# Performance work log

Measured on AMD Instinct MI355X. Metric: run time of the kernel, lower is better.

Reference implementation:

```python
import jax, jax.numpy as jnp
import numpy as np

B, L, V, E = 8, 2000, 50000, 300      # batch, doc len, vocab, embed dim
NL, LW = 8922, 10                     # num labels, words per label desc
F_, K, H = 200, 10, 200               # num_filters, kernel_size, label_hidden
FEAT = E + H                          # feat_size = 500


def setup_inputs():
    key = jax.random.key(0)
    ks = jax.random.split(key, 12)
    n = lambda k, sh, s=0.02: jax.random.normal(k, sh, jnp.float32) * s
    x = jax.random.randint(ks[0], (B, L), 0, V)
    y = (jax.random.uniform(ks[1], (B, NL)) < 0.01).astype(jnp.float32)
    mask = jnp.ones((B, L), jnp.float32)
    word_emb = n(ks[2], (V, E), 0.1)
    label_idx_matrix = jax.random.randint(ks[3], (NL, LW), 0, V)
    label_idx_mask = jnp.ones((NL, LW), jnp.float32)
    adj_matrix = (jax.random.uniform(ks[4], (NL, NL)) < 0.002).astype(jnp.float32)
    num_neighbors = jnp.maximum(adj_matrix.sum(axis=1), 1.0)
    return {
        'x': x, 'y': y, 'mask': mask,
        'word_emb': word_emb,
        'label_idx_matrix': label_idx_matrix,
        'label_idx_mask': label_idx_mask,
        'adj_matrix': adj_matrix,
        'num_neighbors': num_neighbors,
        'Wg': n(ks[5], (E, H)), 'bg': jnp.zeros((H,), jnp.float32),
        'Wc': n(ks[6], (F_, E, K)), 'bc': jnp.zeros((F_,), jnp.float32),
        'Wp': n(ks[7], (F_, E)), 'bp': jnp.zeros((E,), jnp.float32),
        'Wo': n(ks[8], (F_, FEAT)), 'bo': jnp.zeros((FEAT,), jnp.float32),
    }


def reference(x, y, mask, word_emb, label_idx_matrix, label_idx_mask,
              adj_matrix, num_neighbors, Wg, bg, Wc, bc, Wp, bp, Wo, bo):
    # --- average label embedding over label description words ---
    le = word_emb[label_idx_matrix]                              # [NL, LW, E]
    avg = (le * label_idx_mask[..., None]).sum(1)
    avg = avg / label_idx_mask.sum(axis=-1, keepdims=True)       # [NL, E]
    # --- conv graph encoder over label hierarchy ---
    agg = (adj_matrix @ avg) / num_neighbors[:, None]            # [NL, E]
    gh = jax.nn.relu(agg @ Wg + bg)                              # [NL, H]
    graph_emb = jnp.concatenate([avg, gh], axis=-1)              # [NL, FEAT]
    # --- document encoding (dropouts are identity in eval) ---
    xe = word_emb[x] * mask[..., None]                           # [B, L, E]
    c = jax.lax.conv_general_dilated(
        xe.transpose(0, 2, 1), Wc, window_strides=(1,), padding='VALID',
        dimension_numbers=('NCH', 'OIH', 'NCH')) + bc[None, :, None]
    c = jax.nn.relu(c).transpose(0, 2, 1)                        # [B, Lp, F]
    pj = jnp.tanh(c @ Wp + bp)                                   # [B, Lp, E]
    # --- label-wise attention ---
    scores = jnp.einsum('ble,ne->bnl', pj, avg)                  # [B, NL, Lp]
    attn = jax.nn.softmax(scores, axis=-1)
    attn_out = jnp.einsum('bnl,blf->bnf', attn, c)               # [B, NL, F]
    proj = jax.nn.relu(attn_out @ Wo + bo)                       # [B, NL, FEAT]
    logits = (graph_emb[None] * proj).sum(-1)                    # [B, NL]
    # --- BCE-with-logits (sum) / batch ---
    bce = jnp.maximum(logits, 0.0) - logits * y + jnp.log1p(jnp.exp(-jnp.abs(logits)))
    loss = bce.sum() / B
    return (logits, loss)
```

## Files before the change

### kernel.cpp

```cpp
#include <hip/hip_runtime.h>
#include <math.h>

#define B_    8
#define L_    2000
#define V_    50000
#define E_    300
#define NL_   8922
#define NLP_  8960
#define LW_   10
#define F_    200
#define KW_   10
#define H_    200
#define FEAT_ 500
#define LP_   1991

typedef __attribute__((ext_vector_type(8))) short bf16x8;
typedef __attribute__((ext_vector_type(4))) float f32x4;

static __device__ __forceinline__ unsigned short f2b(float f) {
  unsigned u = __builtin_bit_cast(unsigned, f);
  u += 0x7FFF + ((u >> 16) & 1);
  return (unsigned short)(u >> 16);
}
static __device__ __forceinline__ float b2f(unsigned short u) {
  unsigned v = ((unsigned)u) << 16;
  return __builtin_bit_cast(float, v);
}
static __device__ __forceinline__ float fast_tanh(float x) {
  x = fminf(fmaxf(x, -10.f), 10.f);
  float t = __expf(2.f * x);
  return (t - 1.f) / (t + 1.f);
}

#define MFMA(a, b, c) __builtin_amdgcn_mfma_f32_16x16x32_bf16(a, b, c, 0, 0, 0)


__global__ __launch_bounds__(256) void k_avg(const float* __restrict__ we,
                                             const int* __restrict__ lidx,
                                             const float* __restrict__ lmask,
                                             float* __restrict__ avg,
                                             unsigned short* __restrict__ avgb,
                                             unsigned short* __restrict__ geb) {
  int idx = blockIdx.x * 256 + threadIdx.x;
  if (idx >= NLP_ * 80) return;
  int n = idx / 80, e4 = idx - n * 80;
  if (n >= NL_ || e4 >= 75) {
    *(ushort4*)&avgb[(size_t)n * 320 + e4 * 4] = make_ushort4(0, 0, 0, 0);
    return;
  }
  float ax = 0.f, ay = 0.f, az = 0.f, aw = 0.f, ms = 0.f;
#pragma unroll
  for (int w = 0; w < LW_; ++w) {
    float mw = lmask[n * LW_ + w];
    const float4 f = *(const float4*)&we[(size_t)lidx[n * LW_ + w] * E_ + e4 * 4];
    ax = fmaf(f.x, mw, ax); ay = fmaf(f.y, mw, ay);
    az = fmaf(f.z, mw, az); aw = fmaf(f.w, mw, aw);
    ms += mw;
  }
  float inv = 1.f / ms;
  float4 v = {ax * inv, ay * inv, az * inv, aw * inv};
  *(float4*)&avg[(size_t)n * 300 + e4 * 4] = v;
  ushort4 ub = make_ushort4(f2b(v.x), f2b(v.y), f2b(v.z), f2b(v.w));
  *(ushort4*)&avgb[(size_t)n * 320 + e4 * 4] = ub;
  *(ushort4*)&geb[(size_t)n * 512 + e4 * 4] = ub;
}

__global__ __launch_bounds__(256) void k_agg(const float* __restrict__ adj,
                                             const float* __restrict__ avg,
                                             const float* __restrict__ nnb,
                                             float* __restrict__ agg) {
  __shared__ int s_idx[1024];
  __shared__ float s_val[1024];
  __shared__ int s_cnt;
  const int n = blockIdx.x;
  const int tid = threadIdx.x;
  if (tid == 0) s_cnt = 0;
  __syncthreads();
  const float* row = adj + (size_t)n * NL_;
  for (int j = tid; j < NL_; j += 256) {
    float v = row[j];
    if (v != 0.f) {
      int p = atomicAdd(&s_cnt, 1);
      if (p < 1024) { s_idx[p] = j; s_val[p] = v; }
    }
  }
  __syncthreads();
  const int m = min(s_cnt, 1024);
  const float inv = 1.f / nnb[n];
  float a0 = 0.f, a1 = 0.f;
  for (int i = 0; i < m; ++i) {
    const float* ar = avg + (size_t)s_idx[i] * 300;
    float v = s_val[i];
    a0 = fmaf(v, ar[tid], a0);
    if (tid < E_ - 256) a1 = fmaf(v, ar[tid + 256], a1);
  }
  agg[(size_t)n * E_ + tid] = a0 * inv;
  if (tid < E_ - 256) agg[(size_t)n * E_ + tid + 256] = a1 * inv;
}

__global__ __launch_bounds__(256) void k_gh(const float* __restrict__ agg,
                                            const float* __restrict__ Wg,
                                            const float* __restrict__ bg,
                                            unsigned short* __restrict__ geb) {
  __shared__ float s_agg[2400];
  const int n0 = blockIdx.x * 8;
  const int tid = threadIdx.x;
  for (int i = tid; i < 2400; i += 256) {
    int e = i >> 3, nn = i & 7;
    int n = n0 + nn;
    s_agg[i] = (n < NL_) ? agg[(size_t)n * E_ + e] : 0.f;
  }
  __syncthreads();
  if (tid < 96) {
    int nn = tid / 12, c = tid - nn * 12;
    int n = n0 + nn;
    if (n < NL_) geb[(size_t)n * 512 + 500 + c] = 0;
  }
  if (tid < H_) {
    const int h = tid;
    float bb = bg[h];
    float acc[8];
#pragma unroll
    for (int i = 0; i < 8; ++i) acc[i] = bb;
    for (int e = 0; e < E_; ++e) {
      float w = Wg[(size_t)e * H_ + h];
      float4 a0 = *(const float4*)&s_agg[e * 8];
      float4 a1 = *(const float4*)&s_agg[e * 8 + 4];
      acc[0] = fmaf(a0.x, w, acc[0]); acc[1] = fmaf(a0.y, w, acc[1]);
      acc[2] = fmaf(a0.z, w, acc[2]); acc[3] = fmaf(a0.w, w, acc[3]);
      acc[4] = fmaf(a1.x, w, acc[4]); acc[5] = fmaf(a1.y, w, acc[5]);
      acc[6] = fmaf(a1.z, w, acc[6]); acc[7] = fmaf(a1.w, w, acc[7]);
    }
#pragma unroll
    for (int i = 0; i < 8; ++i) {
      int n = n0 + i;
      if (n < NL_) geb[(size_t)n * 512 + 300 + h] = f2b(fmaxf(acc[i], 0.f));
    }
  }
}

__global__ __launch_bounds__(256) void k_wct(const float* __restrict__ Wc,
                                             unsigned short* __restrict__ WcF) {
  int idx = blockIdx.x * 256 + threadIdx.x;
  if (idx >= KW_ * 16 * 10 * 512) return;
  int koff = idx / (16 * 10 * 512);
  int rem = idx - koff * (16 * 10 * 512);
  int ft = rem / (10 * 512);
  int rem2 = rem - ft * (10 * 512);
  int ks = rem2 >> 9;
  int t = rem2 & 511;
  int lane = t >> 3, j = t & 7;
  int f = ft * 16 + (lane & 15);
  int e = ks * 32 + (lane >> 4) * 8 + j;
  float v = (f < F_ && e < E_) ? Wc[((size_t)f * E_ + e) * KW_ + koff] : 0.f;
  WcF[idx] = f2b(v);
}

__global__ __launch_bounds__(256) void k_wpt(const float* __restrict__ Wp,
                                             unsigned short* __restrict__ WpF) {
  int idx = blockIdx.x * 256 + threadIdx.x;
  if (idx >= 20 * 7 * 512) return;
  int et = idx / (7 * 512);
  int rem = idx - et * (7 * 512);
  int kt = rem >> 9;
  int t = rem & 511;
  int lane = t >> 3, j = t & 7;
  int e = et * 16 + (lane & 15);
  int f = kt * 32 + (lane >> 4) * 8 + j;
  float v = (e < E_ && f < F_) ? Wp[(size_t)f * E_ + e] : 0.f;
  WpF[idx] = f2b(v);
}

__global__ __launch_bounds__(256) void k_wot(const float* __restrict__ Wo,
                                             unsigned short* __restrict__ WoF) {
  int idx = blockIdx.x * 256 + threadIdx.x;
  if (idx >= 32 * 7 * 512) return;
  int g = idx / (7 * 512);
  int rem = idx - g * (7 * 512);
  int kt = rem >> 9;
  int t = rem & 511;
  int lane = t >> 3, j = t & 7;
  int feat = (g >> 3) * 128 + (g & 7) * 16 + (lane & 15);
  int f = kt * 32 + (lane >> 4) * 8 + j;
  float v = (feat < FEAT_ && f < F_) ? Wo[(size_t)f * FEAT_ + feat] : 0.f;
  WoF[idx] = f2b(v);
}

__global__ __launch_bounds__(256) void k_cpj(const int* __restrict__ x,
                                             const float* __restrict__ mask,
                                             const float* __restrict__ we,
                                             const unsigned short* __restrict__ WcF,
                                             const float* __restrict__ bc,
                                             const unsigned short* __restrict__ WpF,
                                             const float* __restrict__ bp,
                                             unsigned short* __restrict__ cF,
                                             unsigned short* __restrict__ pjF) {
  __shared__ __attribute__((aligned(16))) unsigned char smem[78896];
  unsigned short* s_xe  = (unsigned short*)smem;
  unsigned short* s_pjF = (unsigned short*)smem;
  unsigned short* s_cA  = (unsigned short*)(smem + 50224);

  const int b = blockIdx.y;
  const int l0 = blockIdx.x * 64;
  const int tid = threadIdx.x;
  const int wv = tid >> 6, lane = tid & 63, quad = lane >> 4, c16 = lane & 15;

  for (int i = tid; i < 73 * 75; i += 256) {
    int row = i / 75, e4 = i - row * 75;
    int l = l0 + row;
    float4 v = {0.f, 0.f, 0.f, 0.f};
    if (l < L_) {
      int bl = b * L_ + l;
      v = *(const float4*)&we[(size_t)x[bl] * E_ + e4 * 4];
      float mm = mask[bl];
      v.x *= mm; v.y *= mm; v.z *= mm; v.w *= mm;
    }
    *(ushort4*)&s_xe[row * 344 + e4 * 4] =
        make_ushort4(f2b(v.x), f2b(v.y), f2b(v.z), f2b(v.w));
  }
  for (int i = tid; i < 73 * 5; i += 256) {
    int row = i / 5, c = i - row * 5;
    *(ushort4*)&s_xe[row * 344 + (75 + c) * 4] = make_ushort4(0, 0, 0, 0);
  }
  __syncthreads();

  f32x4 acc[4][4];
#pragma unroll
  for (int mt = 0; mt < 4; ++mt)
#pragma unroll
    for (int j = 0; j < 4; ++j) acc[mt][j] = (f32x4){0.f, 0.f, 0.f, 0.f};
  for (int koff = 0; koff < KW_; ++koff) {
#pragma unroll
    for (int ks = 0; ks < 10; ++ks) {
      bf16x8 a[4];
#pragma unroll
      for (int mt = 0; mt < 4; ++mt)
        a[mt] = *(const bf16x8*)&s_xe[(mt * 16 + c16 + koff) * 344 + ks * 32 + quad * 8];
#pragma unroll
      for (int jj = 0; jj < 4; ++jj) {
        bf16x8 bw = *(const bf16x8*)
            &WcF[(((size_t)((koff * 16 + wv * 4 + jj) * 10 + ks)) << 9) + (lane << 3)];
#pragma unroll
        for (int mt = 0; mt < 4; ++mt) acc[mt][jj] = MFMA(a[mt], bw, acc[mt][jj]);
      }
    }
  }
  unsigned short* cFb = cF + (size_t)b * (16 * 64 * 512);
#pragma unroll
  for (int jj = 0; jj < 4; ++jj) {
    const int ft2 = wv * 4 + jj;
    const int f = ft2 * 16 + c16;
    const float bcv = (f < F_) ? bc[f] : 0.f;
    const int kt = ft2 >> 1;
    const int qA = ((ft2 & 1) << 1) | (c16 >> 3);
    const int jA = c16 & 7;
#pragma unroll
    for (int mt = 0; mt < 4; ++mt) {
      unsigned short u[4];
#pragma unroll
      for (int r = 0; r < 4; ++r) u[r] = f2b(fmaxf(acc[mt][jj][r] + bcv, 0.f));
      int su = (l0 >> 5) + (mt >> 1);
      int lane_c = ((((mt & 1) << 1) | (quad >> 1)) << 4) + c16;
      *(ushort4*)&cFb[(((size_t)(ft2 * 64 + su)) << 9) + lane_c * 8 + ((quad & 1) << 2)] =
          make_ushort4(u[0], u[1], u[2], u[3]);
      if (ft2 < 14) {
#pragma unroll
        for (int r = 0; r < 4; ++r)
          s_cA[(((size_t)(mt * 7 + kt)) << 9) + ((qA << 4) + quad * 4 + r) * 8 + jA] = u[r];
      }
    }
  }
  __syncthreads();

  f32x4 pacc[4][5];
#pragma unroll
  for (int mt = 0; mt < 4; ++mt)
#pragma unroll
    for (int j = 0; j < 5; ++j) pacc[mt][j] = (f32x4){0.f, 0.f, 0.f, 0.f};
#pragma unroll
  for (int kt = 0; kt < 7; ++kt) {
    bf16x8 a[4];
#pragma unroll
    for (int mt = 0; mt < 4; ++mt)
      a[mt] = *(const bf16x8*)&s_cA[(((size_t)(mt * 7 + kt)) << 9) + (lane << 3)];
#pragma unroll
    for (int j = 0; j < 5; ++j) {
      bf16x8 bw = *(const bf16x8*)
          &WpF[(((size_t)((wv * 5 + j) * 7 + kt)) << 9) + (lane << 3)];
#pragma unroll
      for (int mt = 0; mt < 4; ++mt) pacc[mt][j] = MFMA(a[mt], bw, pacc[mt][j]);
    }
  }
  __syncthreads();
#pragma unroll
  for (int j = 0; j < 5; ++j) {
    const int et = wv * 5 + j;
    const int e = et * 16 + c16;
    const float bpe = (e < E_) ? bp[e] : 0.f;
    const int ks = et >> 1;
    const int qP = ((et & 1) << 1) | (c16 >> 3);
    const int jP = c16 & 7;
#pragma unroll
    for (int mt = 0; mt < 4; ++mt) {
#pragma unroll
      for (int r = 0; r < 4; ++r) {
        float v = (e < E_) ? fast_tanh(pacc[mt][j][r] + bpe) : 0.f;
        s_pjF[(((size_t)(mt * 10 + ks)) << 9) + ((qP << 4) + quad * 4 + r) * 8 + jP] = f2b(v);
      }
    }
  }
  __syncthreads();
  {
    unsigned short* dst = pjF + (((size_t)((b * 128 + (l0 >> 4)) * 10)) << 9);
    for (int i = tid; i < 2560; i += 256)
      *(uint4*)&dst[i * 8] = *(const uint4*)&s_pjF[i * 8];
  }
}

__global__ __launch_bounds__(256, 2) void k_attn(
    const unsigned short* __restrict__ pjF,
    const unsigned short* __restrict__ cF,
    const unsigned short* __restrict__ avgb,
    const unsigned short* __restrict__ WoF,
    const unsigned short* __restrict__ geb,
    const float* __restrict__ bo,
    float* __restrict__ out) {
  __shared__ __attribute__((aligned(16))) unsigned char smem[58880];
  unsigned short* s_avgF = (unsigned short*)smem;
  unsigned short* s_AOF  = (unsigned short*)smem;
  unsigned short* s_PF   = (unsigned short*)(smem + 40960);
  float* s_wsum = (float*)(smem + 57344);
  float* s_sum  = (float*)(smem + 58368);
  float* s_lg   = (float*)(smem + 58624);

  const int tid = threadIdx.x;
  const int b  = blockIdx.x & 7;
  const int n0 = (blockIdx.x >> 3) << 6;
  const int wv = tid >> 6, lane = tid & 63, quad = lane >> 4, c16 = lane & 15;

  if (tid < 64) s_lg[tid] = 0.f;
  for (int i = tid; i < 2560; i += 256) {
    int nl = i / 40, eo = i - nl * 40;
    int lane_s = ((eo & 3) << 4) | (nl & 15);
    *(uint4*)&s_avgF[(((size_t)((eo >> 2) * 4 + (nl >> 4))) << 9) + lane_s * 8] =
        *(const uint4*)&avgb[(size_t)(n0 + nl) * 320 + eo * 8];
  }
  __syncthreads();

  const unsigned short* pjb = pjF + (size_t)b * (128 * 10 * 512);
  const unsigned short* cFb = cF + (size_t)b * (16 * 64 * 512);

  f32x4 o[4][4];
#pragma unroll
  for (int i = 0; i < 4; ++i)
#pragma unroll
    for (int j = 0; j < 4; ++j) o[i][j] = (f32x4){0.f, 0.f, 0.f, 0.f};
  float ssum[4] = {0.f, 0.f, 0.f, 0.f};

  for (int lc = 0; lc < 16; ++lc) {
    f32x4 accs[2][4];
#pragma unroll
    for (int mt = 0; mt < 2; ++mt)
#pragma unroll
      for (int nt = 0; nt < 4; ++nt) accs[mt][nt] = (f32x4){0.f, 0.f, 0.f, 0.f};
    {
      const unsigned short* pr =
          pjb + (((size_t)((lc * 8 + wv * 2) * 10)) << 9) + (lane << 3);
#pragma unroll
      for (int ks = 0; ks < 10; ++ks) {
        bf16x8 a0 = *(const bf16x8*)(pr + ((size_t)ks << 9));
        bf16x8 a1 = *(const bf16x8*)(pr + ((size_t)(10 + ks) << 9));
#pragma unroll
        for (int nt = 0; nt < 4; ++nt) {
          bf16x8 bb = *(const bf16x8*)&s_avgF[(((size_t)(ks * 4 + nt)) << 9) + (lane << 3)];
          accs[0][nt] = MFMA(a0, bb, accs[0][nt]);
          accs[1][nt] = MFMA(a1, bb, accs[1][nt]);
        }
      }
    }
    __syncthreads();
#pragma unroll
    for (int nt = 0; nt < 4; ++nt) {
      float psum = 0.f;
#pragma unroll
      for (int mt = 0; mt < 2; ++mt) {
        const int lb = (lc << 7) + wv * 32 + mt * 16 + quad * 4;
        unsigned short u[4];
#pragma unroll
        for (int r = 0; r < 4; ++r) {
          float p = (lb + r < LP_) ? __expf(accs[mt][nt][r]) : 0.f;
          psum += p;
          u[r] = f2b(p);
        }
        int lane_P = (((mt << 1) | (quad >> 1)) << 4) + c16;
        *(ushort4*)&s_PF[(((size_t)(nt * 4 + wv)) << 9) + lane_P * 8 + ((quad & 1) << 2)] =
            make_ushort4(u[0], u[1], u[2], u[3]);
      }
      psum += __shfl_xor(psum, 16);
      psum += __shfl_xor(psum, 32);
      ssum[nt] += psum;
    }
    __syncthreads();
    {
      const unsigned short* cw =
          cFb + (((size_t)(wv * 4 * 64 + lc * 4)) << 9) + (lane << 3);
#pragma unroll
      for (int sub = 0; sub < 4; ++sub) {
        bf16x8 ap[4];
#pragma unroll
        for (int nt = 0; nt < 4; ++nt)
          ap[nt] = *(const bf16x8*)&s_PF[(((size_t)(nt * 4 + sub)) << 9) + (lane << 3)];
#pragma unroll
        for (int ft = 0; ft < 4; ++ft) {
          bf16x8 bb = *(const bf16x8*)(cw + (((size_t)(ft * 64 + sub)) << 9));
#pragma unroll
          for (int nt = 0; nt < 4; ++nt) o[nt][ft] = MFMA(ap[nt], bb, o[nt][ft]);
        }
      }
    }
  }

  if (lane < 16) {
#pragma unroll
    for (int nt = 0; nt < 4; ++nt) s_wsum[wv * 64 + nt * 16 + lane] = ssum[nt];
  }
  __syncthreads();
  if (tid < 64)
    s_sum[tid] = s_wsum[tid] + s_wsum[64 + tid] + s_wsum[128 + tid] + s_wsum[192 + tid];
  __syncthreads();
#pragma unroll
  for (int nt = 0; nt < 4; ++nt) {
    float inv4[4];
#pragma unroll
    for (int r = 0; r < 4; ++r) inv4[r] = 1.f / s_sum[nt * 16 + quad * 4 + r];
#pragma unroll
    for (int ft = 0; ft < 4; ++ft) {
      int f = wv * 64 + ft * 16 + c16;
      if (f < 224) {
        int kt = f >> 5;
        int qA = (f & 31) >> 3;
        int jA = f & 7;
#pragma unroll
        for (int r = 0; r < 4; ++r)
          s_AOF[(((size_t)(nt * 7 + kt)) << 9) + ((qA << 4) + quad * 4 + r) * 8 + jA] =
              f2b(o[nt][ft][r] * inv4[r]);
      }
    }
  }
  __syncthreads();
  float la[4][4];
#pragma unroll
  for (int nt = 0; nt < 4; ++nt)
#pragma unroll
    for (int r = 0; r < 4; ++r) la[nt][r] = 0.f;
#pragma unroll
  for (int i = 0; i < 8; ++i) {
    f32x4 pa[4];
#pragma unroll
    for (int nt = 0; nt < 4; ++nt) pa[nt] = (f32x4){0.f, 0.f, 0.f, 0.f};
    const unsigned short* wof = WoF + (((size_t)((wv * 8 + i) * 7)) << 9) + (lane << 3);
#pragma unroll
    for (int kt = 0; kt < 7; ++kt) {
      bf16x8 bw = *(const bf16x8*)(wof + ((size_t)kt << 9));
#pragma unroll
      for (int nt = 0; nt < 4; ++nt) {
        bf16x8 aa = *(const bf16x8*)&s_AOF[(((size_t)(nt * 7 + kt)) << 9) + (lane << 3)];
        pa[nt] = MFMA(aa, bw, pa[nt]);
      }
    }
    int feat = wv * 128 + i * 16 + c16;
    float bof = (feat < FEAT_) ? bo[feat] : 0.f;
#pragma unroll
    for (int nt = 0; nt < 4; ++nt) {
#pragma unroll
      for (int r = 0; r < 4; ++r) {
        int ng = n0 + nt * 16 + quad * 4 + r;
        float pv = fmaxf(pa[nt][r] + bof, 0.f);
        float gv = (feat < FEAT_) ? b2f(geb[(size_t)ng * 512 + feat]) : 0.f;
        la[nt][r] = fmaf(pv, gv, la[nt][r]);
      }
    }
  }
#pragma unroll
  for (int nt = 0; nt < 4; ++nt)
#pragma unroll
    for (int r = 0; r < 4; ++r) {
      float v = la[nt][r];
      v += __shfl_xor(v, 1); v += __shfl_xor(v, 2);
      v += __shfl_xor(v, 4); v += __shfl_xor(v, 8);
      if (c16 == 0) atomicAdd(&s_lg[nt * 16 + quad * 4 + r], v);
    }
  __syncthreads();
  if (tid < 64) {
    int ng = n0 + tid;
    if (ng < NL_) out[(size_t)b * NL_ + ng] = s_lg[tid];
  }
}

__global__ __launch_bounds__(1024) void k_loss(const float* __restrict__ lgts,
                                               const float* __restrict__ y,
                                               float* __restrict__ loss) {
  __shared__ float red[1024];
  const int tid = threadIdx.x;
  float s = 0.f;
  for (int i = tid; i < B_ * NL_; i += 1024) {
    float l = lgts[i], yy = y[i];
    s += fmaxf(l, 0.f) - l * yy + log1pf(expf(-fabsf(l)));
  }
  red[tid] = s;
  __syncthreads();
  for (int st = 512; st > 0; st >>= 1) {
    if (tid < st) red[tid] += red[tid + st];
    __syncthreads();
  }
  if (tid == 0) loss[0] = red[0] * (1.f / B_);
}

extern "C" void kernel_launch(void* const* d_in, const int* in_sizes, int n_in,
                              void* d_out, int out_size, void* d_ws, size_t ws_size,
                              hipStream_t stream) {
  const int*   x     = (const int*)  d_in[0];
  const float* y     = (const float*)d_in[1];
  const float* mask  = (const float*)d_in[2];
  const float* we    = (const float*)d_in[3];
  const int*   lidx  = (const int*)  d_in[4];
  const float* lmask = (const float*)d_in[5];
  const float* adj   = (const float*)d_in[6];
  const float* nnb   = (const float*)d_in[7];
  const float* Wg    = (const float*)d_in[8];
  const float* bg    = (const float*)d_in[9];
  const float* Wc    = (const float*)d_in[10];
  const float* bc    = (const float*)d_in[11];
  const float* Wp    = (const float*)d_in[12];
  const float* bp    = (const float*)d_in[13];
  const float* Wo    = (const float*)d_in[14];
  const float* bo    = (const float*)d_in[15];
  float* out = (float*)d_out;
  char* W = (char*)d_ws;

  unsigned short* pjF  = (unsigned short*)(W + 0);
  unsigned short* cF   = (unsigned short*)(W + 10485760);
  unsigned short* avgb = (unsigned short*)(W + 18874368);
  unsigned short* geb  = (unsigned short*)(W + 24608768);
  float*          agg  = (float*)(W + 33783808);
  unsigned short* WcF  = (unsigned short*)(W + 44490208);
  unsigned short* WpF  = (unsigned short*)(W + 46128608);
  unsigned short* WoF  = (unsigned short*)(W + 46271968);
  float*          avg  = (float*)(W + 0);

  k_avg<<<(NLP_ * 80 + 255) / 256, 256, 0, stream>>>(we, lidx, lmask, avg, avgb, geb);
  k_agg<<<NL_, 256, 0, stream>>>(adj, avg, nnb, agg);
  k_gh<<<(NL_ + 7) / 8, 256, 0, stream>>>(agg, Wg, bg, geb);
  k_wct<<<(KW_ * 16 * 10 * 512 + 255) / 256, 256, 0, stream>>>(Wc, WcF);
  k_wpt<<<(20 * 7 * 512 + 255) / 256, 256, 0, stream>>>(Wp, WpF);
  k_wot<<<(32 * 7 * 512 + 255) / 256, 256, 0, stream>>>(Wo, WoF);
  k_cpj<<<dim3(32, B_), 256, 0, stream>>>(x, mask, we, WcF, bc, WpF, bp, cF, pjF);
  k_attn<<<140 * 8, 256, 0, stream>>>(pjF, cF, avgb, WoF, geb, bo, out);
  k_loss<<<1, 1024, 0, stream>>>(out, y, out + B_ * NL_);
}
```

Baseline: 1.237 ms.

## Restructure attention kernel with double-buffered LDS staging and per-wave label tiles

The attention kernel is reorganized so each wave owns 16 labels across the full feature width. The label-embedding operand is now held in registers instead of LDS. The pj and c tiles for each 32-position chunk are brought into LDS with global_load_lds, double-buffered so the next chunk loads while the current one is computed. The graph-embedding buffer gets an MFMA-fragment-friendly layout, so the epilogue reads it with one vector load per tile instead of scattered scalar loads. This also needs a memset of that buffer and matching index changes in k_avg, k_gh and k_wot. The aim is to remove redundant global reads and the cross-wave syncs, at the cost of more registers (14 accumulator tiles), more LDS, and a full-buffer waitcnt barrier every iteration.

```diff
diff --git a/kernel.cpp b/kernel.cpp
--- a/kernel.cpp
+++ b/kernel.cpp
@@ -31,6 +31,11 @@
   float t = __expf(2.f * x);
   return (t - 1.f) / (t + 1.f);
 }
+static __device__ __forceinline__ void stage16(const void* g, void* l) {
+  __builtin_amdgcn_global_load_lds(
+      (const __attribute__((address_space(1))) unsigned int*)g,
+      (__attribute__((address_space(3))) unsigned int*)l, 16, 0, 0);
+}
 
 #define MFMA(a, b, c) __builtin_amdgcn_mfma_f32_16x16x32_bf16(a, b, c, 0, 0, 0)
 
@@ -40,7 +45,7 @@
                                              const float* __restrict__ lmask,
                                              float* __restrict__ avg,
                                              unsigned short* __restrict__ avgb,
-                                             unsigned short* __restrict__ geb) {
+                                             unsigned short* __restrict__ geF) {
   int idx = blockIdx.x * 256 + threadIdx.x;
   if (idx >= NLP_ * 80) return;
   int n = idx / 80, e4 = idx - n * 80;
@@ -60,9 +65,15 @@
   float inv = 1.f / ms;
   float4 v = {ax * inv, ay * inv, az * inv, aw * inv};
   *(float4*)&avg[(size_t)n * 300 + e4 * 4] = v;
-  ushort4 ub = make_ushort4(f2b(v.x), f2b(v.y), f2b(v.z), f2b(v.w));
-  *(ushort4*)&avgb[(size_t)n * 320 + e4 * 4] = ub;
-  *(ushort4*)&geb[(size_t)n * 512 + e4 * 4] = ub;
+  *(ushort4*)&avgb[(size_t)n * 320 + e4 * 4] =
+      make_ushort4(f2b(v.x), f2b(v.y), f2b(v.z), f2b(v.w));
+  int ntg = n >> 4, quad = (n >> 2) & 3, r = n & 3;
+  int ftg = (e4 * 4) >> 4, c0 = (e4 * 4) & 15;
+  size_t tb = (((size_t)ntg * 32 + ftg) << 8);
+  float vv[4] = {v.x, v.y, v.z, v.w};
+#pragma unroll
+  for (int t = 0; t < 4; ++t)
+    geF[(tb + quad * 16 + c0 + t) * 4 + r] = f2b(vv[t]);
 }
 
 __global__ __launch_bounds__(256) void k_agg(const float* __restrict__ adj,
@@ -101,7 +112,7 @@
 __global__ __launch_bounds__(256) void k_gh(const float* __restrict__ agg,
                                             const float* __restrict__ Wg,
                                             const float* __restrict__ bg,
-                                            unsigned short* __restrict__ geb) {
+                                            unsigned short* __restrict__ geF) {
   __shared__ float s_agg[2400];
   const int n0 = blockIdx.x * 8;
   const int tid = threadIdx.x;
@@ -111,13 +122,9 @@
     s_agg[i] = (n < NL_) ? agg[(size_t)n * E_ + e] : 0.f;
   }
   __syncthreads();
-  if (tid < 96) {
-    int nn = tid / 12, c = tid - nn * 12;
-    int n = n0 + nn;
-    if (n < NL_) geb[(size_t)n * 512 + 500 + c] = 0;
-  }
   if (tid < H_) {
     const int h = tid;
+    const int feat = 300 + h;
     float bb = bg[h];
     float acc[8];
 #pragma unroll
@@ -131,10 +138,14 @@
       acc[4] = fmaf(a1.x, w, acc[4]); acc[5] = fmaf(a1.y, w, acc[5]);
       acc[6] = fmaf(a1.z, w, acc[6]); acc[7] = fmaf(a1.w, w, acc[7]);
     }
+    const int ftg = feat >> 4, cc = feat & 15;
 #pragma unroll
     for (int i = 0; i < 8; ++i) {
       int n = n0 + i;
-      if (n < NL_) geb[(size_t)n * 512 + 300 + h] = f2b(fmaxf(acc[i], 0.f));
+      if (n < NL_) {
+        size_t tb = (((size_t)(n >> 4) * 32 + ftg) << 8);
+        geF[(tb + ((n >> 2) & 3) * 16 + cc) * 4 + (n & 3)] = f2b(fmaxf(acc[i], 0.f));
+      }
     }
   }
 }
@@ -180,7 +191,7 @@
   int kt = rem >> 9;
   int t = rem & 511;
   int lane = t >> 3, j = t & 7;
-  int feat = (g >> 3) * 128 + (g & 7) * 16 + (lane & 15);
+  int feat = g * 16 + (lane & 15);
   int f = kt * 32 + (lane >> 4) * 8 + j;
   float v = (feat < FEAT_ && f < F_) ? Wo[(size_t)f * FEAT_ + feat] : 0.f;
   WoF[idx] = f2b(v);
@@ -322,16 +333,14 @@
     const unsigned short* __restrict__ cF,
     const unsigned short* __restrict__ avgb,
     const unsigned short* __restrict__ WoF,
-    const unsigned short* __restrict__ geb,
+    const unsigned short* __restrict__ geF,
     const float* __restrict__ bo,
     float* __restrict__ out) {
-  __shared__ __attribute__((aligned(16))) unsigned char smem[58880];
-  unsigned short* s_avgF = (unsigned short*)smem;
-  unsigned short* s_AOF  = (unsigned short*)smem;
-  unsigned short* s_PF   = (unsigned short*)(smem + 40960);
-  float* s_wsum = (float*)(smem + 57344);
-  float* s_sum  = (float*)(smem + 58368);
-  float* s_lg   = (float*)(smem + 58624);
+  __shared__ __attribute__((aligned(16))) unsigned char smem[74240];
+  unsigned short* Ps  = (unsigned short*)(smem + 69632);
+  float* s_sum = (float*)(smem + 73728);
+  float* s_lg  = (float*)(smem + 73984);
+  unsigned short* AOs = (unsigned short*)smem;
 
   const int tid = threadIdx.x;
   const int b  = blockIdx.x & 7;
@@ -339,145 +348,147 @@
   const int wv = tid >> 6, lane = tid & 63, quad = lane >> 4, c16 = lane & 15;
 
   if (tid < 64) s_lg[tid] = 0.f;
-  for (int i = tid; i < 2560; i += 256) {
-    int nl = i / 40, eo = i - nl * 40;
-    int lane_s = ((eo & 3) << 4) | (nl & 15);
-    *(uint4*)&s_avgF[(((size_t)((eo >> 2) * 4 + (nl >> 4))) << 9) + lane_s * 8] =
-        *(const uint4*)&avgb[(size_t)(n0 + nl) * 320 + eo * 8];
-  }
-  __syncthreads();
+
+  bf16x8 bavg[10];
+  {
+    const unsigned short* ab = avgb + (size_t)(n0 + wv * 16 + c16) * 320 + quad * 8;
+#pragma unroll
+    for (int ks = 0; ks < 10; ++ks) bavg[ks] = *(const bf16x8*)(ab + ks * 32);
+  }
 
   const unsigned short* pjb = pjF + (size_t)b * (128 * 10 * 512);
   const unsigned short* cFb = cF + (size_t)b * (16 * 64 * 512);
 
-  f32x4 o[4][4];
-#pragma unroll
-  for (int i = 0; i < 4; ++i)
-#pragma unroll
-    for (int j = 0; j < 4; ++j) o[i][j] = (f32x4){0.f, 0.f, 0.f, 0.f};
-  float ssum[4] = {0.f, 0.f, 0.f, 0.f};
-
-  for (int lc = 0; lc < 16; ++lc) {
-    f32x4 accs[2][4];
-#pragma unroll
-    for (int mt = 0; mt < 2; ++mt)
-#pragma unroll
-      for (int nt = 0; nt < 4; ++nt) accs[mt][nt] = (f32x4){0.f, 0.f, 0.f, 0.f};
+  {
+    const unsigned char* pg = (const unsigned char*)pjb;
+#pragma unroll
+    for (int t = 0; t < 5; ++t) {
+      int off = (wv * 5 + t) << 10;
+      stage16(pg + off + lane * 16, smem + off);
+    }
+#pragma unroll
+    for (int t = 0; t < 4; ++t) {
+      int ft = wv + t * 4;
+      if (ft < 14)
+        stage16((const unsigned char*)cFb + (((size_t)(ft * 64)) << 10) + lane * 16,
+                smem + 20480 + (ft << 10));
+    }
+  }
+
+  f32x4 o[14];
+#pragma unroll
+  for (int i = 0; i < 14; ++i) o[i] = (f32x4){0.f, 0.f, 0.f, 0.f};
+  float ssum = 0.f;
+
+  for (int lc = 0; lc < 64; ++lc) {
+    __builtin_amdgcn_s_waitcnt(0);
+    __syncthreads();
+    unsigned char* cur = smem + ((lc & 1) ? 34816 : 0);
+    unsigned char* nxt = smem + ((lc & 1) ? 0 : 34816);
+    if (lc + 1 < 64) {
+      const unsigned char* pg =
+          (const unsigned char*)pjb + (((size_t)((lc + 1) * 20)) << 10);
+#pragma unroll
+      for (int t = 0; t < 5; ++t) {
+        int off = (wv * 5 + t) << 10;
+        stage16(pg + off + lane * 16, nxt + off);
+      }
+#pragma unroll
+      for (int t = 0; t < 4; ++t) {
+        int ft = wv + t * 4;
+        if (ft < 14)
+          stage16((const unsigned char*)cFb + (((size_t)(ft * 64 + lc + 1)) << 10) + lane * 16,
+                  nxt + 20480 + (ft << 10));
+      }
+    }
+    const unsigned short* pt = (const unsigned short*)cur;
+    f32x4 acc0 = (f32x4){0.f, 0.f, 0.f, 0.f};
+    f32x4 acc1 = (f32x4){0.f, 0.f, 0.f, 0.f};
+#pragma unroll
+    for (int ks = 0; ks < 10; ++ks) {
+      bf16x8 a0 = *(const bf16x8*)(pt + (ks << 9) + (lane << 3));
+      bf16x8 a1 = *(const bf16x8*)(pt + ((10 + ks) << 9) + (lane << 3));
+      acc0 = MFMA(a0, bavg[ks], acc0);
+      acc1 = MFMA(a1, bavg[ks], acc1);
+    }
+    float psum = 0.f;
+#pragma unroll
+    for (int lt = 0; lt < 2; ++lt) {
+      f32x4 av = lt ? acc1 : acc0;
+      int lb = (lc << 5) + lt * 16 + quad * 4;
+      unsigned short u[4];
+#pragma unroll
+      for (int r = 0; r < 4; ++r) {
+        float p = (lb + r < LP_) ? __expf(av[r]) : 0.f;
+        psum += p;
+        u[r] = f2b(p);
+      }
+      *(ushort4*)&Ps[(wv << 9) + (((lt * 2 + (quad >> 1)) * 16 + c16) << 3) +
+                     ((quad & 1) << 2)] = make_ushort4(u[0], u[1], u[2], u[3]);
+    }
+    psum += __shfl_xor(psum, 16);
+    psum += __shfl_xor(psum, 32);
+    ssum += psum;
     {
-      const unsigned short* pr =
-          pjb + (((size_t)((lc * 8 + wv * 2) * 10)) << 9) + (lane << 3);
-#pragma unroll
-      for (int ks = 0; ks < 10; ++ks) {
-        bf16x8 a0 = *(const bf16x8*)(pr + ((size_t)ks << 9));
-        bf16x8 a1 = *(const bf16x8*)(pr + ((size_t)(10 + ks) << 9));
-#pragma unroll
-        for (int nt = 0; nt < 4; ++nt) {
-          bf16x8 bb = *(const bf16x8*)&s_avgF[(((size_t)(ks * 4 + nt)) << 9) + (lane << 3)];
-          accs[0][nt] = MFMA(a0, bb, accs[0][nt]);
-          accs[1][nt] = MFMA(a1, bb, accs[1][nt]);
-        }
-      }
-    }
-    __syncthreads();
+      bf16x8 aP = *(const bf16x8*)&Ps[(wv << 9) + (lane << 3)];
+      const unsigned short* cc = (const unsigned short*)(cur + 20480);
+#pragma unroll
+      for (int ft = 0; ft < 14; ++ft) {
+        bf16x8 bC = *(const bf16x8*)(cc + (ft << 9) + (lane << 3));
+        o[ft] = MFMA(aP, bC, o[ft]);
+      }
+    }
+  }
+
+  if (lane < 16) s_sum[wv * 16 + lane] = ssum;
+  {
+    float inv4[4];
+#pragma unroll
+    for (int r = 0; r < 4; ++r) inv4[r] = 1.f / s_sum[wv * 16 + quad * 4 + r];
+#pragma unroll
+    for (int ft = 0; ft < 14; ++ft) {
+      int kt = ft >> 1;
+      int quadA = ((ft & 1) << 1) | (c16 >> 3);
+      int jA = c16 & 7;
+#pragma unroll
+      for (int r = 0; r < 4; ++r)
+        AOs[wv * 3584 + (kt << 9) + (quadA * 16 + quad * 4 + r) * 8 + jA] =
+            f2b(o[ft][r] * inv4[r]);
+    }
+  }
+  __syncthreads();
+  float la[4][4];
+#pragma unroll
+  for (int nt = 0; nt < 4; ++nt)
+#pragma unroll
+    for (int r = 0; r < 4; ++r) la[nt][r] = 0.f;
+#pragma unroll
+  for (int i = 0; i < 8; ++i) {
+    const int ftg = wv * 8 + i;
+    const int feat = (ftg << 4) + c16;
+    f32x4 pa[4];
+#pragma unroll
+    for (int nt = 0; nt < 4; ++nt) pa[nt] = (f32x4){0.f, 0.f, 0.f, 0.f};
+    const unsigned short* wof = WoF + (((size_t)(ftg * 7)) << 9) + (lane << 3);
+#pragma unroll
+    for (int kt = 0; kt < 7; ++kt) {
+      bf16x8 bw = *(const bf16x8*)(wof + (kt << 9));
+#pragma unroll
+      for (int nt = 0; nt < 4; ++nt) {
+        bf16x8 aa = *(const bf16x8*)&AOs[nt * 3584 + (kt << 9) + (lane << 3)];
+        pa[nt] = MFMA(aa, bw, pa[nt]);
+      }
+    }
+    const float bof = (feat < FEAT_) ? bo[feat] : 0.f;
 #pragma unroll
     for (int nt = 0; nt < 4; ++nt) {
-      float psum = 0.f;
-#pragma unroll
-      for (int mt = 0; mt < 2; ++mt) {
-        const int lb = (lc << 7) + wv * 32 + mt * 16 + quad * 4;
-        unsigned short u[4];
-#pragma unroll
-        for (int r = 0; r < 4; ++r) {
-          float p = (lb + r < LP_) ? __expf(accs[mt][nt][r]) : 0.f;
-          psum += p;
-          u[r] = f2b(p);
-        }
-        int lane_P = (((mt << 1) | (quad >> 1)) << 4) + c16;
-        *(ushort4*)&s_PF[(((size_t)(nt * 4 + wv)) << 9) + lane_P * 8 + ((quad & 1) << 2)] =
-            make_ushort4(u[0], u[1], u[2], u[3]);
-      }
-      psum += __shfl_xor(psum, 16);
-      psum += __shfl_xor(psum, 32);
-      ssum[nt] += psum;
-    }
-    __syncthreads();
-    {
-      const unsigned short* cw =
-          cFb + (((size_t)(wv * 4 * 64 + lc * 4)) << 9) + (lane << 3);
-#pragma unroll
-      for (int sub = 0; sub < 4; ++sub) {
-        bf16x8 ap[4];
-#pragma unroll
-        for (int nt = 0; nt < 4; ++nt)
-          ap[nt] = *(const bf16x8*)&s_PF[(((size_t)(nt * 4 + sub)) << 9) + (lane << 3)];
-#pragma unroll
-        for (int ft = 0; ft < 4; ++ft) {
-          bf16x8 bb = *(const bf16x8*)(cw + (((size_t)(ft * 64 + sub)) << 9));
-#pragma unroll
-          for (int nt = 0; nt < 4; ++nt) o[nt][ft] = MFMA(ap[nt], bb, o[nt][ft]);
-        }
-      }
-    }
-  }
-
-  if (lane < 16) {
-#pragma unroll
-    for (int nt = 0; nt < 4; ++nt) s_wsum[wv * 64 + nt * 16 + lane] = ssum[nt];
-  }
-  __syncthreads();
-  if (tid < 64)
-    s_sum[tid] = s_wsum[tid] + s_wsum[64 + tid] + s_wsum[128 + tid] + s_wsum[192 + tid];
-  __syncthreads();
-#pragma unroll
-  for (int nt = 0; nt < 4; ++nt) {
-    float inv4[4];
-#pragma unroll
-    for (int r = 0; r < 4; ++r) inv4[r] = 1.f / s_sum[nt * 16 + quad * 4 + r];
-#pragma unroll
-    for (int ft = 0; ft < 4; ++ft) {
-      int f = wv * 64 + ft * 16 + c16;
-      if (f < 224) {
-        int kt = f >> 5;
-        int qA = (f & 31) >> 3;
-        int jA = f & 7;
-#pragma unroll
-        for (int r = 0; r < 4; ++r)
-          s_AOF[(((size_t)(nt * 7 + kt)) << 9) + ((qA << 4) + quad * 4 + r) * 8 + jA] =
-              f2b(o[nt][ft][r] * inv4[r]);
-      }
-    }
-  }
-  __syncthreads();
-  float la[4][4];
-#pragma unroll
-  for (int nt = 0; nt < 4; ++nt)
-#pragma unroll
-    for (int r = 0; r < 4; ++r) la[nt][r] = 0.f;
-#pragma unroll
-  for (int i = 0; i < 8; ++i) {
-    f32x4 pa[4];
-#pragma unroll
-    for (int nt = 0; nt < 4; ++nt) pa[nt] = (f32x4){0.f, 0.f, 0.f, 0.f};
-    const unsigned short* wof = WoF + (((size_t)((wv * 8 + i) * 7)) << 9) + (lane << 3);
-#pragma unroll
-    for (int kt = 0; kt < 7; ++kt) {
-      bf16x8 bw = *(const bf16x8*)(wof + ((size_t)kt << 9));
-#pragma unroll
-      for (int nt = 0; nt < 4; ++nt) {
-        bf16x8 aa = *(const bf16x8*)&s_AOF[(((size_t)(nt * 7 + kt)) << 9) + (lane << 3)];
-        pa[nt] = MFMA(aa, bw, pa[nt]);
-      }
-    }
-    int feat = wv * 128 + i * 16 + c16;
-    float bof = (feat < FEAT_) ? bo[feat] : 0.f;
-#pragma unroll
-    for (int nt = 0; nt < 4; ++nt) {
+      ushort4 g4 = *(const ushort4*)
+          &geF[((((size_t)(n0 >> 4) + nt) * 32 + ftg) << 8) + (lane << 2)];
+      float gv[4] = {b2f(g4.x), b2f(g4.y), b2f(g4.z), b2f(g4.w)};
 #pragma unroll
       for (int r = 0; r < 4; ++r) {
-        int ng = n0 + nt * 16 + quad * 4 + r;
         float pv = fmaxf(pa[nt][r] + bof, 0.f);
-        float gv = (feat < FEAT_) ? b2f(geb[(size_t)ng * 512 + feat]) : 0.f;
-        la[nt][r] = fmaf(pv, gv, la[nt][r]);
+        la[nt][r] = fmaf(pv, gv[r], la[nt][r]);
       }
     }
   }
@@ -541,20 +552,21 @@
   unsigned short* pjF  = (unsigned short*)(W + 0);
   unsigned short* cF   = (unsigned short*)(W + 10485760);
   unsigned short* avgb = (unsigned short*)(W + 18874368);
-  unsigned short* geb  = (unsigned short*)(W + 24608768);
+  unsigned short* geF  = (unsigned short*)(W + 24608768);
   float*          agg  = (float*)(W + 33783808);
   unsigned short* WcF  = (unsigned short*)(W + 44490208);
   unsigned short* WpF  = (unsigned short*)(W + 46128608);
   unsigned short* WoF  = (unsigned short*)(W + 46271968);
   float*          avg  = (float*)(W + 0);
 
-  k_avg<<<(NLP_ * 80 + 255) / 256, 256, 0, stream>>>(we, lidx, lmask, avg, avgb, geb);
+  hipMemsetAsync(geF, 0, 9175040, stream);
+  k_avg<<<(NLP_ * 80 + 255) / 256, 256, 0, stream>>>(we, lidx, lmask, avg, avgb, geF);
   k_agg<<<NL_, 256, 0, stream>>>(adj, avg, nnb, agg);
-  k_gh<<<(NL_ + 7) / 8, 256, 0, stream>>>(agg, Wg, bg, geb);
+  k_gh<<<(NL_ + 7) / 8, 256, 0, stream>>>(agg, Wg, bg, geF);
   k_wct<<<(KW_ * 16 * 10 * 512 + 255) / 256, 256, 0, stream>>>(Wc, WcF);
   k_wpt<<<(20 * 7 * 512 + 255) / 256, 256, 0, stream>>>(Wp, WpF);
   k_wot<<<(32 * 7 * 512 + 255) / 256, 256, 0, stream>>>(Wo, WoF);
   k_cpj<<<dim3(32, B_), 256, 0, stream>>>(x, mask, we, WcF, bc, WpF, bp, cF, pjF);
-  k_attn<<<140 * 8, 256, 0, stream>>>(pjF, cF, avgb, WoF, geb, bo, out);
+  k_attn<<<140 * 8, 256, 0, stream>>>(pjF, cF, avgb, WoF, geF, bo, out);
   k_loss<<<1, 1024, 0, stream>>>(out, y, out + B_ * NL_);
 }
```

Measured after the change: 1.030 ms. -16.7%, faster.
